# Optimization experiments

Hardware: AMD Instinct MI355X
Metric: run time of the kernel (lower is better)

The kernel has to match this reference:

```python
import jax, jax.numpy as jnp
import numpy as np

B, N, C, OUT, K2 = 64, 4096, 64, 64, 4  # batch, lattice sites, in/out features, kersize^2

def setup_inputs() -> dict:
    key = jax.random.key(0)
    k1, k2, k3, k4 = jax.random.split(key, 4)
    std = 0.5 / jnp.sqrt(K2 * (C + OUT))  # matches module's init stddev (W_scale=b_scale=1)
    x = jax.random.normal(k1, (B, N, C), dtype=jnp.float32)
    W = jax.random.normal(k2, (K2, C, OUT), dtype=jnp.float32) * std
    b = jax.random.normal(k3, (OUT,), dtype=jnp.float32) * std
    kernel2 = jax.random.randint(k4, (N, K2), 0, N, dtype=jnp.int32)
    return {"x": x, "W": W, "b": b, "kernel2": kernel2}

def reference(x, W, b, kernel2):
    # gather neighbors: [B, N, K2, C]; contract (K2, C) with W -> [B, N, OUT]
    y = jnp.einsum('bnkc,kco->bno', x[:, kernel2, :], W)
    # bias broadcast (original used tensordot with ones([B,N]))
    return y + b
```

## Files before the change

### kernel.cpp

```cpp
#include <hip/hip_runtime.h>
#include <stdint.h>


#define N_SITES  4096
#define C_DIM    64
#define OUT_DIM  64

typedef __attribute__((ext_vector_type(8))) short bf16x8;
typedef __attribute__((ext_vector_type(4))) float f32x4;

__device__ __forceinline__ uint32_t pack2_bf16(float f0, float f1) {
    uint32_t u0 = __float_as_uint(f0) + 0x8000u;
    uint32_t u1 = __float_as_uint(f1) + 0x8000u;
    return __builtin_amdgcn_perm(u1, u0, 0x07060302u);
}

template<int N> __device__ __forceinline__ void wait_vmcnt() {
    asm volatile("s_waitcnt vmcnt(%0)" :: "n"(N) : "memory");
}

__device__ __forceinline__ void gll16(const float* p, uint32_t m0v) {
    asm volatile("s_mov_b32 m0, %1\n\t"
                 "global_load_lds_dwordx4 %0, off"
                 :: "v"(p), "s"(m0v) : "memory");
}

__global__ __launch_bounds__(64, 1)
void conv_async_kernel(const float* __restrict__ x, const float* __restrict__ W,
                       const float* __restrict__ bias, const int* __restrict__ kernel2,
                       float* __restrict__ out)
{
    __shared__ __align__(1024) uint8_t lds_raw[33280];

    const int lane = threadIdx.x;
    const int bi   = blockIdx.x;
    const int half = bi >> 10;
    const int r    = bi & 1023;
    const int bgl  = r & 7;
    const int sg   = r >> 3;
    const int bg   = bgl + half * 8;
    const int n0   = sg * 32;
    const int b0   = bg * 4;

    const int c  = lane & 15;
    const int q  = lane >> 4;
    const int sl = c >> 2;
    const int bb = c & 3;

    if (lane < 32) {
        int4 iv = ((const int4*)kernel2)[n0 + lane];
        *(int4*)(lds_raw + 32768 + lane * 16) = iv;
    }

    bf16x8 aw[4][8];
    #pragma unroll
    for (int t = 0; t < 4; ++t)
        #pragma unroll
        for (int s = 0; s < 8; ++s) {
            uint32_t* ap = (uint32_t*)&aw[t][s];
            #pragma unroll
            for (int u = 0; u < 4; ++u) {
                float f0 = W[(size_t)(s*32 + q*8 + 2*u    ) * OUT_DIM + t*16 + c];
                float f1 = W[(size_t)(s*32 + q*8 + 2*u + 1) * OUT_DIM + t*16 + c];
                ap[u] = pack2_bf16(f0, f1);
            }
        }

    f32x4 bias_r[4];
    #pragma unroll
    for (int t = 0; t < 4; ++t) bias_r[t] = *(const f32x4*)&bias[t*16 + q*4];

    const float* gx = x + (size_t)(b0 + bb) * (N_SITES * C_DIM) + q * 4;

    const uint32_t lds0 =
        __builtin_amdgcn_readfirstlane((uint32_t)(uintptr_t)lds_raw);

    wait_vmcnt<0>();

    auto issue_ht = [&](int i) {
        const uint8_t* ib = lds_raw + 32768 + (i >> 1) * 64 + (i & 1) * 8;
        int2 iv0 = *(const int2*)(ib);
        int2 iv1 = *(const int2*)(ib + 16);
        int2 iv2 = *(const int2*)(ib + 32);
        int2 iv3 = *(const int2*)(ib + 48);
        const uint32_t m0b = lds0 + (uint32_t)(i & 3) * 8192;
        #pragma unroll
        for (int kl = 0; kl < 2; ++kl) {
            const int e0 = kl ? iv0.y : iv0.x;
            const int e1 = kl ? iv1.y : iv1.x;
            const int e2 = kl ? iv2.y : iv2.x;
            const int e3 = kl ? iv3.y : iv3.x;
            const int nk = (sl & 2) ? ((sl & 1) ? e3 : e2)
                                    : ((sl & 1) ? e1 : e0);
            const float* row = gx + (size_t)(uint32_t)nk * C_DIM;
            gll16(row,      m0b + (uint32_t)(kl*4 + 0) * 1024);
            gll16(row + 16, m0b + (uint32_t)(kl*4 + 1) * 1024);
            gll16(row + 32, m0b + (uint32_t)(kl*4 + 2) * 1024);
            gll16(row + 48, m0b + (uint32_t)(kl*4 + 3) * 1024);
        }
    };

    auto comp_ht = [&](int i, f32x4* acc) {
        const uint32_t tb = (uint32_t)(i & 3) * 8192;
        const int hb = (i & 1) * 4;
        #pragma unroll
        for (int s = 0; s < 4; ++s) {
            const uint8_t* pb = lds_raw + tb + s*2048 + q*512 + c*16;
            f32x4 xa = *(const f32x4*)(pb);
            f32x4 xb = *(const f32x4*)(pb + 256);
            bf16x8 bf;
            uint32_t* bp = (uint32_t*)&bf;
            bp[0] = pack2_bf16(xa[0], xa[1]);
            bp[1] = pack2_bf16(xa[2], xa[3]);
            bp[2] = pack2_bf16(xb[0], xb[1]);
            bp[3] = pack2_bf16(xb[2], xb[3]);
            #pragma unroll
            for (int t = 0; t < 4; ++t)
                acc[t] = __builtin_amdgcn_mfma_f32_16x16x32_bf16(aw[t][hb + s], bf, acc[t], 0, 0, 0);
        }
    };

    issue_ht(0);
    issue_ht(1);
    issue_ht(2);
    issue_ht(3);

    #pragma unroll
    for (int p = 0; p < 8; ++p) {
        f32x4 acc[4];
        #pragma unroll
        for (int t = 0; t < 4; ++t) acc[t] = (f32x4){0.f, 0.f, 0.f, 0.f};

        if      (p == 0) wait_vmcnt<24>();
        else if (p == 1) wait_vmcnt<28>();
        else if (p == 7) wait_vmcnt<16>();
        else             wait_vmcnt<32>();
        comp_ht(2*p, acc);
        if (p <= 5) issue_ht(2*p + 4);

        if      (p == 0) wait_vmcnt<24>();
        else if (p == 1) wait_vmcnt<28>();
        else if (p == 6) wait_vmcnt<24>();
        else if (p == 7) wait_vmcnt<8>();
        else             wait_vmcnt<32>();
        comp_ht(2*p + 1, acc);
        if (p <= 5) issue_ht(2*p + 5);

        const int n = n0 + p*4 + sl;
        float* op = out + ((size_t)(b0 + bb) * N_SITES + n) * OUT_DIM + q*4;
        #pragma unroll
        for (int t = 0; t < 4; ++t)
            *(f32x4*)(op + t*16) = acc[t] + bias_r[t];
    }
}

extern "C" void kernel_launch(void* const* d_in, const int* in_sizes, int n_in,
                              void* d_out, int out_size, void* d_ws, size_t ws_size,
                              hipStream_t stream) {
    const float* x       = (const float*)d_in[0];
    const float* W       = (const float*)d_in[1];
    const float* bias    = (const float*)d_in[2];
    const int*   kernel2 = (const int*)d_in[3];
    float* out = (float*)d_out;

    conv_async_kernel<<<2048, 64, 0, stream>>>(x, W, bias, kernel2, out);
}
```

Measured before the change: 147.1 us.

## Remap gather loads so each lane group fetches contiguous rows with XOR-swizzled LDS

Changes the gather mapping so the 16 lanes of a group load one full 256-byte row of a neighbor site for one batch, instead of each lane loading 16-byte chunks scattered across four rows. The LDS layout becomes row-major per site with an XOR swizzle on 32-byte chunks, and the compute reads are adjusted to match. The aim is more coalesced global memory transactions for the gathered rows and fewer LDS bank conflicts on the reads. Per half-tile the load count stays the same (8 gll16). The risk is a mismatch between the swizzle used when writing and when reading, which would make results wrong.

```diff
diff --git a/kernel.cpp b/kernel.cpp
--- a/kernel.cpp
+++ b/kernel.cpp
@@ -47,6 +47,9 @@
     const int sl = c >> 2;
     const int bb = c & 3;
 
+    const int g  = lane >> 4;
+    const int u  = lane & 15;
+
     if (lane < 32) {
         int4 iv = ((const int4*)kernel2)[n0 + lane];
         *(int4*)(lds_raw + 32768 + lane * 16) = iv;
@@ -59,10 +62,10 @@
         for (int s = 0; s < 8; ++s) {
             uint32_t* ap = (uint32_t*)&aw[t][s];
             #pragma unroll
-            for (int u = 0; u < 4; ++u) {
-                float f0 = W[(size_t)(s*32 + q*8 + 2*u    ) * OUT_DIM + t*16 + c];
-                float f1 = W[(size_t)(s*32 + q*8 + 2*u + 1) * OUT_DIM + t*16 + c];
-                ap[u] = pack2_bf16(f0, f1);
+            for (int uu = 0; uu < 4; ++uu) {
+                float f0 = W[(size_t)(s*32 + q*8 + 2*uu    ) * OUT_DIM + t*16 + c];
+                float f1 = W[(size_t)(s*32 + q*8 + 2*uu + 1) * OUT_DIM + t*16 + c];
+                ap[uu] = pack2_bf16(f0, f1);
             }
         }
 
@@ -70,7 +73,8 @@
     #pragma unroll
     for (int t = 0; t < 4; ++t) bias_r[t] = *(const f32x4*)&bias[t*16 + q*4];
 
-    const float* gx = x + (size_t)(b0 + bb) * (N_SITES * C_DIM) + q * 4;
+    const float* gxn = x + (size_t)(b0 + g) * (N_SITES * C_DIM)
+                     + (size_t)((((u >> 1) ^ g) * 8) + (u & 1) * 4);
 
     const uint32_t lds0 =
         __builtin_amdgcn_readfirstlane((uint32_t)(uintptr_t)lds_raw);
@@ -78,25 +82,17 @@
     wait_vmcnt<0>();
 
     auto issue_ht = [&](int i) {
-        const uint8_t* ib = lds_raw + 32768 + (i >> 1) * 64 + (i & 1) * 8;
-        int2 iv0 = *(const int2*)(ib);
-        int2 iv1 = *(const int2*)(ib + 16);
-        int2 iv2 = *(const int2*)(ib + 32);
-        int2 iv3 = *(const int2*)(ib + 48);
-        const uint32_t m0b = lds0 + (uint32_t)(i & 3) * 8192;
+        const int pp = i >> 1, h = i & 1;
+        const int* ibase = (const int*)(lds_raw + 32768 + pp * 64);
+        const uint32_t m0s = lds0 + (uint32_t)(i & 3) * 8192;
         #pragma unroll
         for (int kl = 0; kl < 2; ++kl) {
-            const int e0 = kl ? iv0.y : iv0.x;
-            const int e1 = kl ? iv1.y : iv1.x;
-            const int e2 = kl ? iv2.y : iv2.x;
-            const int e3 = kl ? iv3.y : iv3.x;
-            const int nk = (sl & 2) ? ((sl & 1) ? e3 : e2)
-                                    : ((sl & 1) ? e1 : e0);
-            const float* row = gx + (size_t)(uint32_t)nk * C_DIM;
-            gll16(row,      m0b + (uint32_t)(kl*4 + 0) * 1024);
-            gll16(row + 16, m0b + (uint32_t)(kl*4 + 1) * 1024);
-            gll16(row + 32, m0b + (uint32_t)(kl*4 + 2) * 1024);
-            gll16(row + 48, m0b + (uint32_t)(kl*4 + 3) * 1024);
+            #pragma unroll
+            for (int slp = 0; slp < 4; ++slp) {
+                const int nk = ibase[slp * 4 + 2 * h + kl];
+                const float* row = gxn + (size_t)(uint32_t)nk * C_DIM;
+                gll16(row, m0s + (uint32_t)kl * 4096 + (uint32_t)slp * 1024);
+            }
         }
     };
 
@@ -104,10 +100,14 @@
         const uint32_t tb = (uint32_t)(i & 3) * 8192;
         const int hb = (i & 1) * 4;
         #pragma unroll
-        for (int s = 0; s < 4; ++s) {
-            const uint8_t* pb = lds_raw + tb + s*2048 + q*512 + c*16;
+        for (int kl = 0; kl < 2; ++kl)
+        #pragma unroll
+        for (int hs = 0; hs < 2; ++hs) {
+            const uint8_t* pb = lds_raw + tb + (uint32_t)kl * 4096
+                              + (uint32_t)c * 256
+                              + (uint32_t)((((hs * 4 + q) ^ (c & 3)) * 32));
             f32x4 xa = *(const f32x4*)(pb);
-            f32x4 xb = *(const f32x4*)(pb + 256);
+            f32x4 xb = *(const f32x4*)(pb + 16);
             bf16x8 bf;
             uint32_t* bp = (uint32_t*)&bf;
             bp[0] = pack2_bf16(xa[0], xa[1]);
@@ -116,7 +116,8 @@
             bp[3] = pack2_bf16(xb[2], xb[3]);
             #pragma unroll
             for (int t = 0; t < 4; ++t)
-                acc[t] = __builtin_amdgcn_mfma_f32_16x16x32_bf16(aw[t][hb + s], bf, acc[t], 0, 0, 0);
+                acc[t] = __builtin_amdgcn_mfma_f32_16x16x32_bf16(
+                    aw[t][hb + kl * 2 + hs], bf, acc[t], 0, 0, 0);
         }
     };
 
```

After: 137.0 us. 1.07x faster.
